# Kernel optimization log

Hardware: AMD Instinct MI355X
Metric: run time of the kernel (lower is better)

## Reference

```python
import jax, jax.numpy as jnp
import numpy as np

N, E, D, T = 50000, 500000, 128, 4
EPS = 1e-5


def setup_inputs() -> dict:
    key = jax.random.key(0)
    ks = jax.random.split(key, 14)
    s = 1.0 / np.sqrt(D)
    return {
        "x": jax.random.normal(ks[0], (N, D), jnp.float32),
        "edge_index": jax.random.randint(ks[1], (2, E), 0, N, jnp.int32),
        "edge_type": jax.random.randint(ks[2], (E,), 0, T, jnp.int32),
        "edge_features": jax.random.normal(ks[3], (E, D), jnp.float32),
        # per-edge-type linear transforms (torch Linear equiv, [in, out] layout)
        "W_types": jax.random.uniform(ks[4], (T, D, D), jnp.float32, -s, s),
        "b_types": jax.random.uniform(ks[5], (T, D), jnp.float32, -s, s),
        # self-loop transform (BaseGNNLayer.transform)
        "W_self": jax.random.uniform(ks[6], (D, D), jnp.float32, -s, s),
        "b_self": jax.random.uniform(ks[7], (D,), jnp.float32, -s, s),
        # edge_processor MLP: Linear(D, D) -> ReLU -> Linear(D, D)
        "W_e1": jax.random.uniform(ks[8], (D, D), jnp.float32, -s, s),
        "b_e1": jax.random.uniform(ks[9], (D,), jnp.float32, -s, s),
        "W_e2": jax.random.uniform(ks[10], (D, D), jnp.float32, -s, s),
        "b_e2": jax.random.uniform(ks[11], (D,), jnp.float32, -s, s),
        # LayerNorm params
        "ln_g": jnp.ones((D,), jnp.float32),
        "ln_b": jnp.zeros((D,), jnp.float32),
    }


def reference(x, edge_index, edge_type, edge_features,
              W_types, b_types, W_self, b_self,
              W_e1, b_e1, W_e2, b_e2, ln_g, ln_b):
    row, col = edge_index[0], edge_index[1]
    x_col = x[col]  # [E, D] gather of source-node features
    num_types = W_types.shape[0]
    # per-edge-type linear transform, selected by edge_type mask
    msgs = jnp.zeros((x_col.shape[0], W_types.shape[2]), x.dtype)
    for t in range(num_types):  # small fixed loop over edge types
        m_t = x_col @ W_types[t] + b_types[t]
        msgs = msgs + jnp.where((edge_type == t)[:, None], m_t, jnp.zeros((), x.dtype))
    # edge-feature MLP, added once per edge (each edge has exactly one type)
    ep = jax.nn.relu(edge_features @ W_e1 + b_e1) @ W_e2 + b_e2
    msgs = msgs + ep
    # scatter-add messages to destination nodes
    out = jax.ops.segment_sum(msgs, row, num_segments=x.shape[0])
    # self loops via the base transform
    out = out + x @ W_self + b_self
    # LayerNorm over feature dim
    mu = jnp.mean(out, axis=-1, keepdims=True)
    var = jnp.mean(jnp.square(out - mu), axis=-1, keepdims=True)
    out = (out - mu) * jax.lax.rsqrt(var + EPS) * ln_g + ln_b
    return jax.nn.relu(out)
```

## Files before the change

### kernel.cpp

```cpp
#include <hip/hip_runtime.h>

#define Nn 50000
#define Ee 500000
#define Dd 128

typedef __attribute__((ext_vector_type(8))) short bf16x8;
typedef __attribute__((ext_vector_type(4))) float f32x4;

__device__ inline unsigned short f2bf(float f) {
  unsigned u = __float_as_uint(f);
  unsigned r = u + 0x7FFFu + ((u >> 16) & 1u);
  return (unsigned short)(r >> 16);
}

__global__ __launch_bounds__(256) void prep_kernel(
    const float* __restrict__ x, const float* __restrict__ W_types,
    const float* __restrict__ b_types, const float* __restrict__ W_self,
    const float* __restrict__ W_e1, const float* __restrict__ W_e2,
    const float* __restrict__ b_e2,
    unsigned short* __restrict__ xbf, unsigned short* __restrict__ WTt,
    unsigned short* __restrict__ W1T, unsigned short* __restrict__ W2T,
    unsigned short* __restrict__ WsT, float* __restrict__ biasc) {
  int i = blockIdx.x * 256 + threadIdx.x;
  if (i < 65536) {
    int t = i >> 14, rem = i & 16383, n = rem >> 7, k = rem & 127;
    WTt[i] = f2bf(W_types[t * 16384 + k * 128 + n]);
  } else if (i < 81920) {
    int j = i - 65536; int n = j >> 7, k = j & 127;
    W1T[j] = f2bf(W_e1[k * 128 + n]);
  } else if (i < 98304) {
    int j = i - 81920; int n = j >> 7, k = j & 127;
    W2T[j] = f2bf(W_e2[k * 128 + n]);
  } else if (i < 114688) {
    int j = i - 98304; int n = j >> 7, k = j & 127;
    WsT[j] = f2bf(W_self[k * 128 + n]);
  } else if (i < 115200) {
    int j = i - 114688; int n = j & 127;
    biasc[j] = b_types[j] + b_e2[n];
  } else if (i < 115200 + Nn * Dd) {
    int j = i - 115200;
    xbf[j] = f2bf(x[j]);
  }
}

__global__ __launch_bounds__(256) void hist_kernel(const int* __restrict__ et,
                                                   int* __restrict__ hist) {
  __shared__ int h[4];
  if (threadIdx.x < 4) h[threadIdx.x] = 0;
  __syncthreads();
  for (int i = blockIdx.x * 256 + threadIdx.x; i < Ee; i += gridDim.x * 256)
    atomicAdd(&h[et[i]], 1);
  __syncthreads();
  if (threadIdx.x < 4) atomicAdd(&hist[threadIdx.x], h[threadIdx.x]);
}

__global__ void prefix_kernel(const int* __restrict__ hist, int* __restrict__ cursor) {
  if (threadIdx.x == 0) {
    int s = 0;
    for (int t = 0; t < 4; ++t) { cursor[t] = s; s += hist[t]; }
  }
}

__global__ __launch_bounds__(256) void scatter_kernel(const int* __restrict__ et,
                                                      int* __restrict__ cursor,
                                                      int* __restrict__ sorted_eid) {
  __shared__ int lc[4], bb[4];
  if (threadIdx.x < 4) lc[threadIdx.x] = 0;
  __syncthreads();
  int per = (Ee + gridDim.x - 1) / gridDim.x;
  int s = blockIdx.x * per;
  int e = min(Ee, s + per);
  for (int i = s + (int)threadIdx.x; i < e; i += 256) atomicAdd(&lc[et[i]], 1);
  __syncthreads();
  if (threadIdx.x < 4) bb[threadIdx.x] = atomicAdd(&cursor[threadIdx.x], lc[threadIdx.x]);
  __syncthreads();
  if (threadIdx.x < 4) lc[threadIdx.x] = bb[threadIdx.x];
  __syncthreads();
  for (int i = s + (int)threadIdx.x; i < e; i += 256) {
    int p = atomicAdd(&lc[et[i]], 1);
    sorted_eid[p] = i;
  }
}

__device__ inline void stageW(const unsigned short* __restrict__ Wg,
                              unsigned short* __restrict__ Wb, int tid) {
  const uint4* src = (const uint4*)Wg;
#pragma unroll
  for (int c = 0; c < 8; ++c) {
    int ch = c * 256 + tid;
    int row = ch >> 4;
    int off = (ch & 15) << 4;
    *(uint4*)((char*)Wb + row * 256 + (off ^ ((row & 7) << 4))) = src[ch];
  }
}

__global__ __launch_bounds__(256, 3) void edge_kernel(
    const int* __restrict__ edge_index, const int* __restrict__ edge_type,
    const float* __restrict__ ef, const unsigned short* __restrict__ xbf,
    const unsigned short* __restrict__ WTt, const unsigned short* __restrict__ W1T,
    const unsigned short* __restrict__ W2T, const float* __restrict__ biasc,
    const float* __restrict__ b_e1, const int* __restrict__ sorted_eid,
    float* __restrict__ accum) {
  __shared__ __align__(16) unsigned short Wb[16384];
  __shared__ unsigned short Hs[64][136];
  __shared__ int mrow[64];
  __shared__ int mtype[64];
  __shared__ int tmask_s;

  const int tid = threadIdx.x;
  const int tile0 = blockIdx.x * 64;

  if (tid < 64) {
    if (tid == 0) tmask_s = 0;
    int i = tile0 + tid;
    int r = -1, t = -1;
    if (i < Ee) {
      int ee = sorted_eid[i];
      r = edge_index[ee];
      t = edge_type[ee];
    }
    mrow[tid] = r;
    mtype[tid] = t;
    if (t >= 0) atomicOr(&tmask_s, 1 << t);
  }

  const int w = tid >> 6, l = tid & 63, quad = l >> 4, lm = l & 15;
  const int mr = w * 16 + lm;
  const int rswz = (lm & 7) << 4;

  const int i = tile0 + mr;
  const int e = sorted_eid[i < Ee ? i : Ee - 1];
  const int myt = edge_type[e];
  const int colnode = edge_index[Ee + e];

  bf16x8 ax[4];
  {
    const unsigned short* xp = xbf + colnode * Dd + quad * 8;
#pragma unroll
    for (int ks = 0; ks < 4; ++ks) ax[ks] = *(const bf16x8*)(xp + ks * 32);
  }

  stageW(W1T, Wb, tid);
  __syncthreads();

  f32x4 h[8];
#pragma unroll
  for (int c = 0; c < 8; ++c) h[c] = (f32x4){0.f, 0.f, 0.f, 0.f};
  const float* efp = ef + (long long)e * Dd + quad * 8;
#pragma unroll
  for (int ks = 0; ks < 4; ++ks) {
    float4 v0 = *(const float4*)(efp + ks * 32);
    float4 v1 = *(const float4*)(efp + ks * 32 + 4);
    bf16x8 a;
    a[0] = f2bf(v0.x); a[1] = f2bf(v0.y); a[2] = f2bf(v0.z); a[3] = f2bf(v0.w);
    a[4] = f2bf(v1.x); a[5] = f2bf(v1.y); a[6] = f2bf(v1.z); a[7] = f2bf(v1.w);
    const int fb = (ks * 64 + quad * 16) ^ rswz;
#pragma unroll
    for (int c = 0; c < 8; ++c) {
      bf16x8 b = *(const bf16x8*)((const char*)Wb + (c * 16 + lm) * 256 + fb);
      h[c] = __builtin_amdgcn_mfma_f32_16x16x32_bf16(a, b, h[c], 0, 0, 0);
    }
  }
#pragma unroll
  for (int c = 0; c < 8; ++c) {
    int n = c * 16 + lm;
    float be = b_e1[n];
#pragma unroll
    for (int r4 = 0; r4 < 4; ++r4) {
      float v = h[c][r4] + be;
      v = v > 0.f ? v : 0.f;
      Hs[w * 16 + quad * 4 + r4][n] = f2bf(v);
    }
  }
  __syncthreads();

  stageW(W2T, Wb, tid);
  __syncthreads();

  f32x4 msg[8];
#pragma unroll
  for (int c = 0; c < 8; ++c) msg[c] = (f32x4){0.f, 0.f, 0.f, 0.f};

#pragma unroll
  for (int ks = 0; ks < 4; ++ks) {
    bf16x8 a = *(const bf16x8*)&Hs[mr][ks * 32 + quad * 8];
    const int fb = (ks * 64 + quad * 16) ^ rswz;
#pragma unroll
    for (int c = 0; c < 8; ++c) {
      bf16x8 b = *(const bf16x8*)((const char*)Wb + (c * 16 + lm) * 256 + fb);
      msg[c] = __builtin_amdgcn_mfma_f32_16x16x32_bf16(a, b, msg[c], 0, 0, 0);
    }
  }
  __syncthreads();

  const int tmask = tmask_s;
  for (int t = 0; t < 4; ++t) {
    if (!(tmask & (1 << t))) continue;
    stageW(WTt + t * Dd * Dd, Wb, tid);
    __syncthreads();
    bool mine = (myt == t);
    if (__any(mine)) {
#pragma unroll
      for (int ks = 0; ks < 4; ++ks) {
        bf16x8 a = mine ? ax[ks] : (bf16x8){0, 0, 0, 0, 0, 0, 0, 0};
        const int fb = (ks * 64 + quad * 16) ^ rswz;
#pragma unroll
        for (int c = 0; c < 8; ++c) {
          bf16x8 b = *(const bf16x8*)((const char*)Wb + (c * 16 + lm) * 256 + fb);
          msg[c] = __builtin_amdgcn_mfma_f32_16x16x32_bf16(a, b, msg[c], 0, 0, 0);
        }
      }
    }
    __syncthreads();
  }

#pragma unroll
  for (int r4 = 0; r4 < 4; ++r4) {
    int m = w * 16 + quad * 4 + r4;
    int rn = mrow[m];
    if (rn < 0) continue;
    int t = mtype[m];
    float* dst = accum + (long long)rn * Dd;
    const float* bc = biasc + t * Dd;
#pragma unroll
    for (int c = 0; c < 8; ++c) {
      int n = c * 16 + lm;
      unsafeAtomicAdd(dst + n, msg[c][r4] + bc[n]);
    }
  }
}

__global__ __launch_bounds__(256) void selfln_kernel(
    const unsigned short* __restrict__ xbf, const unsigned short* __restrict__ WsT,
    const float* __restrict__ b_self, const float* __restrict__ accum,
    const float* __restrict__ ln_g, const float* __restrict__ ln_b,
    float* __restrict__ out) {
  __shared__ unsigned short Axl[64][136];
  __shared__ float S[64][132];
  __shared__ float P1[64][4], P2[64][4];
  __shared__ float MU[64], RS[64];

  const int tid = threadIdx.x;
  const int tile0 = blockIdx.x * 64;
  {
    const int r = tid >> 2, c0 = (tid & 3) * 32;
    int row = tile0 + r;
    if (row < Nn) {
      const uint4* xs = (const uint4*)(xbf + row * Dd + c0);
      uint4* xd = (uint4*)&Axl[r][c0];
      xd[0] = xs[0]; xd[1] = xs[1]; xd[2] = xs[2]; xd[3] = xs[3];
    } else {
      uint4 z = {0, 0, 0, 0};
      uint4* xd = (uint4*)&Axl[r][c0];
      xd[0] = z; xd[1] = z; xd[2] = z; xd[3] = z;
    }
  }
  __syncthreads();

  const int w = tid >> 6, l = tid & 63, quad = l >> 4, lm = l & 15;
  const int mr = w * 16 + lm;
  f32x4 acc[8];
#pragma unroll
  for (int c = 0; c < 8; ++c) acc[c] = (f32x4){0.f, 0.f, 0.f, 0.f};
#pragma unroll
  for (int ks = 0; ks < 4; ++ks) {
    bf16x8 a = *(const bf16x8*)&Axl[mr][ks * 32 + quad * 8];
#pragma unroll
    for (int c = 0; c < 8; ++c) {
      bf16x8 b = *(const bf16x8*)(WsT + (c * 16 + lm) * Dd + ks * 32 + quad * 8);
      acc[c] = __builtin_amdgcn_mfma_f32_16x16x32_bf16(a, b, acc[c], 0, 0, 0);
    }
  }
#pragma unroll
  for (int c = 0; c < 8; ++c) {
    int n = c * 16 + lm;
    float bs = b_self[n];
#pragma unroll
    for (int r4 = 0; r4 < 4; ++r4) {
      int m = w * 16 + quad * 4 + r4;
      int grow = tile0 + m;
      float v = acc[c][r4] + bs;
      if (grow < Nn) v += accum[(long long)grow * Dd + n];
      S[m][n] = v;
    }
  }
  __syncthreads();
  {
    const int r = tid >> 2, sgi = tid & 3, c0 = sgi * 32;
    float s1 = 0.f, s2 = 0.f;
#pragma unroll
    for (int j = 0; j < 32; ++j) { float v = S[r][c0 + j]; s1 += v; s2 += v * v; }
    P1[r][sgi] = s1; P2[r][sgi] = s2;
  }
  __syncthreads();
  if (tid < 64) {
    float s1 = P1[tid][0] + P1[tid][1] + P1[tid][2] + P1[tid][3];
    float s2 = P2[tid][0] + P2[tid][1] + P2[tid][2] + P2[tid][3];
    float mu = s1 * (1.f / 128.f);
    float var = s2 * (1.f / 128.f) - mu * mu;
    MU[tid] = mu;
    RS[tid] = rsqrtf(var + 1e-5f);
  }
  __syncthreads();
  {
    const int r = tid >> 2, c0 = (tid & 3) * 32;
    int row = tile0 + r;
    if (row < Nn) {
      float mu = MU[r], rs = RS[r];
      float* op = out + (long long)row * Dd + c0;
#pragma unroll
      for (int j = 0; j < 32; ++j) {
        float v = (S[r][c0 + j] - mu) * rs * ln_g[c0 + j] + ln_b[c0 + j];
        op[j] = v > 0.f ? v : 0.f;
      }
    }
  }
}

extern "C" void kernel_launch(void* const* d_in, const int* in_sizes, int n_in,
                              void* d_out, int out_size, void* d_ws, size_t ws_size,
                              hipStream_t stream) {
  (void)in_sizes; (void)n_in; (void)out_size; (void)ws_size;
  const float* x       = (const float*)d_in[0];
  const int*   eidx    = (const int*)d_in[1];
  const int*   etype   = (const int*)d_in[2];
  const float* ef      = (const float*)d_in[3];
  const float* W_types = (const float*)d_in[4];
  const float* b_types = (const float*)d_in[5];
  const float* W_self  = (const float*)d_in[6];
  const float* b_self  = (const float*)d_in[7];
  const float* W_e1    = (const float*)d_in[8];
  const float* b_e1    = (const float*)d_in[9];
  const float* W_e2    = (const float*)d_in[10];
  const float* b_e2    = (const float*)d_in[11];
  const float* ln_g    = (const float*)d_in[12];
  const float* ln_b    = (const float*)d_in[13];
  float* out = (float*)d_out;

  char* ws = (char*)d_ws;
  int*            ints   = (int*)ws;
  float*          accum  = (float*)(ws + 512);
  unsigned short* xbf    = (unsigned short*)(ws + 512 + 25600000);
  unsigned short* WTt    = (unsigned short*)(ws + 512 + 25600000 + 12800000);
  unsigned short* W1T    = WTt + 4 * 128 * 128;
  unsigned short* W2T    = W1T + 128 * 128;
  unsigned short* WsT    = W2T + 128 * 128;
  float*          biasc  = (float*)(WsT + 128 * 128);
  int*            sorted = (int*)((char*)biasc + 2048);

  hipMemsetAsync(ws, 0, 512 + (size_t)Nn * Dd * 4, stream);

  prep_kernel<<<25450, 256, 0, stream>>>(x, W_types, b_types, W_self, W_e1, W_e2,
                                         b_e2, xbf, WTt, W1T, W2T, WsT, biasc);
  hist_kernel<<<512, 256, 0, stream>>>(etype, ints);
  prefix_kernel<<<1, 64, 0, stream>>>(ints, ints + 4);
  scatter_kernel<<<512, 256, 0, stream>>>(etype, ints + 4, sorted);
  edge_kernel<<<(Ee + 63) / 64, 256, 0, stream>>>(eidx, etype, ef, xbf, WTt, W1T,
                                                  W2T, biasc, b_e1, sorted, accum);
  selfln_kernel<<<(Nn + 63) / 64, 256, 0, stream>>>(xbf, WsT, b_self, accum, ln_g,
                                                    ln_b, out);
}
```

Baseline: 700.2 us.

## Keep edge MLP hidden in registers via shuffles; register-only LayerNorm

The edge kernel now computes the first MLP layer transposed, so hidden activations land in a layout that wave shuffles can repack into A-fragments for the second layer. This removes the Hs shared buffer and its store/load round trip, and the edge-feature loads are issued early, before the weight staging. Occupancy bounds are raised from 3 to 4 blocks. The self/LayerNorm kernel moves to 128-thread, 32-row blocks and does the row reductions with in-wave xor shuffles instead of shared-memory passes. The cost is extra register pressure and shuffle instructions in exchange for less LDS traffic and fewer barriers.

Result: faster. 638.3 us (-8.9%).

```diff
diff --git a/kernel.cpp b/kernel.cpp
--- a/kernel.cpp
+++ b/kernel.cpp
@@ -94,7 +94,7 @@
   }
 }
 
-__global__ __launch_bounds__(256, 3) void edge_kernel(
+__global__ __launch_bounds__(256, 4) void edge_kernel(
     const int* __restrict__ edge_index, const int* __restrict__ edge_type,
     const float* __restrict__ ef, const unsigned short* __restrict__ xbf,
     const unsigned short* __restrict__ WTt, const unsigned short* __restrict__ W1T,
@@ -102,7 +102,6 @@
     const float* __restrict__ b_e1, const int* __restrict__ sorted_eid,
     float* __restrict__ accum) {
   __shared__ __align__(16) unsigned short Wb[16384];
-  __shared__ unsigned short Hs[64][136];
   __shared__ int mrow[64];
   __shared__ int mtype[64];
   __shared__ int tmask_s;
@@ -139,56 +138,77 @@
 #pragma unroll
     for (int ks = 0; ks < 4; ++ks) ax[ks] = *(const bf16x8*)(xp + ks * 32);
   }
+  float4 efr[8];
+  {
+    const float* efp = ef + (long long)e * Dd + quad * 8;
+#pragma unroll
+    for (int j = 0; j < 8; ++j)
+      efr[j] = *(const float4*)(efp + (j >> 1) * 32 + (j & 1) * 4);
+  }
 
   stageW(W1T, Wb, tid);
   __syncthreads();
 
-  f32x4 h[8];
-#pragma unroll
-  for (int c = 0; c < 8; ++c) h[c] = (f32x4){0.f, 0.f, 0.f, 0.f};
-  const float* efp = ef + (long long)e * Dd + quad * 8;
+  bf16x8 efrag[4];
 #pragma unroll
   for (int ks = 0; ks < 4; ++ks) {
-    float4 v0 = *(const float4*)(efp + ks * 32);
-    float4 v1 = *(const float4*)(efp + ks * 32 + 4);
+    float4 v0 = efr[2 * ks], v1 = efr[2 * ks + 1];
     bf16x8 a;
     a[0] = f2bf(v0.x); a[1] = f2bf(v0.y); a[2] = f2bf(v0.z); a[3] = f2bf(v0.w);
     a[4] = f2bf(v1.x); a[5] = f2bf(v1.y); a[6] = f2bf(v1.z); a[7] = f2bf(v1.w);
+    efrag[ks] = a;
+  }
+
+  f32x4 h2[8];
+#pragma unroll
+  for (int c = 0; c < 8; ++c) h2[c] = (f32x4){0.f, 0.f, 0.f, 0.f};
+#pragma unroll
+  for (int ks = 0; ks < 4; ++ks) {
     const int fb = (ks * 64 + quad * 16) ^ rswz;
 #pragma unroll
     for (int c = 0; c < 8; ++c) {
-      bf16x8 b = *(const bf16x8*)((const char*)Wb + (c * 16 + lm) * 256 + fb);
-      h[c] = __builtin_amdgcn_mfma_f32_16x16x32_bf16(a, b, h[c], 0, 0, 0);
-    }
-  }
+      bf16x8 wf = *(const bf16x8*)((const char*)Wb + (c * 16 + lm) * 256 + fb);
+      h2[c] = __builtin_amdgcn_mfma_f32_16x16x32_bf16(wf, efrag[ks], h2[c], 0, 0, 0);
+    }
+  }
+  __syncthreads();
+
+  stageW(W2T, Wb, tid);
+
+  int pk[8][2];
 #pragma unroll
   for (int c = 0; c < 8; ++c) {
-    int n = c * 16 + lm;
-    float be = b_e1[n];
-#pragma unroll
-    for (int r4 = 0; r4 < 4; ++r4) {
-      float v = h[c][r4] + be;
-      v = v > 0.f ? v : 0.f;
-      Hs[w * 16 + quad * 4 + r4][n] = f2bf(v);
-    }
-  }
-  __syncthreads();
-
-  stageW(W2T, Wb, tid);
+    float4 be = *(const float4*)(b_e1 + c * 16 + quad * 4);
+    float v0 = h2[c][0] + be.x; v0 = v0 > 0.f ? v0 : 0.f;
+    float v1 = h2[c][1] + be.y; v1 = v1 > 0.f ? v1 : 0.f;
+    float v2 = h2[c][2] + be.z; v2 = v2 > 0.f ? v2 : 0.f;
+    float v3 = h2[c][3] + be.w; v3 = v3 > 0.f ? v3 : 0.f;
+    pk[c][0] = (int)f2bf(v0) | ((int)f2bf(v1) << 16);
+    pk[c][1] = (int)f2bf(v2) | ((int)f2bf(v3) << 16);
+  }
   __syncthreads();
 
   f32x4 msg[8];
 #pragma unroll
   for (int c = 0; c < 8; ++c) msg[c] = (f32x4){0.f, 0.f, 0.f, 0.f};
 
+  const int sa = ((quad & 1) << 5) + lm;
+  const int sb = sa + 16;
+  const bool chi = ((quad >> 1) & 1) != 0;
 #pragma unroll
   for (int ks = 0; ks < 4; ++ks) {
-    bf16x8 a = *(const bf16x8*)&Hs[mr][ks * 32 + quad * 8];
+    int a0 = __shfl(pk[2 * ks][0], sa),     a1 = __shfl(pk[2 * ks][1], sa);
+    int a2 = __shfl(pk[2 * ks][0], sb),     a3 = __shfl(pk[2 * ks][1], sb);
+    int b0 = __shfl(pk[2 * ks + 1][0], sa), b1 = __shfl(pk[2 * ks + 1][1], sa);
+    int b2 = __shfl(pk[2 * ks + 1][0], sb), b3 = __shfl(pk[2 * ks + 1][1], sb);
+    union { int4 i; bf16x8 v; } cv;
+    cv.i = chi ? (int4){b0, b1, b2, b3} : (int4){a0, a1, a2, a3};
+    bf16x8 af = cv.v;
     const int fb = (ks * 64 + quad * 16) ^ rswz;
 #pragma unroll
     for (int c = 0; c < 8; ++c) {
-      bf16x8 b = *(const bf16x8*)((const char*)Wb + (c * 16 + lm) * 256 + fb);
-      msg[c] = __builtin_amdgcn_mfma_f32_16x16x32_bf16(a, b, msg[c], 0, 0, 0);
+      bf16x8 wf = *(const bf16x8*)((const char*)Wb + (c * 16 + lm) * 256 + fb);
+      msg[c] = __builtin_amdgcn_mfma_f32_16x16x32_bf16(af, wf, msg[c], 0, 0, 0);
     }
   }
   __syncthreads();
@@ -230,18 +250,15 @@
   }
 }
 
-__global__ __launch_bounds__(256) void selfln_kernel(
+__global__ __launch_bounds__(128, 4) void selfln_kernel(
     const unsigned short* __restrict__ xbf, const unsigned short* __restrict__ WsT,
     const float* __restrict__ b_self, const float* __restrict__ accum,
     const float* __restrict__ ln_g, const float* __restrict__ ln_b,
     float* __restrict__ out) {
-  __shared__ unsigned short Axl[64][136];
-  __shared__ float S[64][132];
-  __shared__ float P1[64][4], P2[64][4];
-  __shared__ float MU[64], RS[64];
+  __shared__ unsigned short Axl[32][136];
 
   const int tid = threadIdx.x;
-  const int tile0 = blockIdx.x * 64;
+  const int tile0 = blockIdx.x * 32;
   {
     const int r = tid >> 2, c0 = (tid & 3) * 32;
     int row = tile0 + r;
@@ -271,47 +288,47 @@
       acc[c] = __builtin_amdgcn_mfma_f32_16x16x32_bf16(a, b, acc[c], 0, 0, 0);
     }
   }
+
+  float s1[4] = {0.f, 0.f, 0.f, 0.f}, s2[4] = {0.f, 0.f, 0.f, 0.f};
 #pragma unroll
   for (int c = 0; c < 8; ++c) {
     int n = c * 16 + lm;
     float bs = b_self[n];
 #pragma unroll
     for (int r4 = 0; r4 < 4; ++r4) {
-      int m = w * 16 + quad * 4 + r4;
-      int grow = tile0 + m;
+      int grow = tile0 + w * 16 + quad * 4 + r4;
       float v = acc[c][r4] + bs;
       if (grow < Nn) v += accum[(long long)grow * Dd + n];
-      S[m][n] = v;
-    }
-  }
-  __syncthreads();
-  {
-    const int r = tid >> 2, sgi = tid & 3, c0 = sgi * 32;
-    float s1 = 0.f, s2 = 0.f;
-#pragma unroll
-    for (int j = 0; j < 32; ++j) { float v = S[r][c0 + j]; s1 += v; s2 += v * v; }
-    P1[r][sgi] = s1; P2[r][sgi] = s2;
-  }
-  __syncthreads();
-  if (tid < 64) {
-    float s1 = P1[tid][0] + P1[tid][1] + P1[tid][2] + P1[tid][3];
-    float s2 = P2[tid][0] + P2[tid][1] + P2[tid][2] + P2[tid][3];
-    float mu = s1 * (1.f / 128.f);
-    float var = s2 * (1.f / 128.f) - mu * mu;
-    MU[tid] = mu;
-    RS[tid] = rsqrtf(var + 1e-5f);
-  }
-  __syncthreads();
-  {
-    const int r = tid >> 2, c0 = (tid & 3) * 32;
-    int row = tile0 + r;
-    if (row < Nn) {
-      float mu = MU[r], rs = RS[r];
-      float* op = out + (long long)row * Dd + c0;
-#pragma unroll
-      for (int j = 0; j < 32; ++j) {
-        float v = (S[r][c0 + j] - mu) * rs * ln_g[c0 + j] + ln_b[c0 + j];
-        op[j] = v > 0.f ? v : 0.f;
+      acc[c][r4] = v;
+      s1[r4] += v;
+      s2[r4] += v * v;
+    }
+  }
+#pragma unroll
+  for (int off = 1; off < 16; off <<= 1) {
+#pragma unroll
+    for (int r4 = 0; r4 < 4; ++r4) {
+      s1[r4] += __shfl_xor(s1[r4], off);
+      s2[r4] += __shfl_xor(s2[r4], off);
+    }
+  }
+  float mu[4], rs[4];
+#pragma unroll
+  for (int r4 = 0; r4 < 4; ++r4) {
+    mu[r4] = s1[r4] * (1.f / 128.f);
+    float var = s2[r4] * (1.f / 128.f) - mu[r4] * mu[r4];
+    rs[r4] = rsqrtf(var + 1e-5f);
+  }
+#pragma unroll
+  for (int c = 0; c < 8; ++c) {
+    int n = c * 16 + lm;
+    float g = ln_g[n], bb = ln_b[n];
+#pragma unroll
+    for (int r4 = 0; r4 < 4; ++r4) {
+      int grow = tile0 + w * 16 + quad * 4 + r4;
+      if (grow < Nn) {
+        float v = (acc[c][r4] - mu[r4]) * rs[r4] * g + bb;
+        out[(long long)grow * Dd + n] = v > 0.f ? v : 0.f;
       }
     }
   }
@@ -357,6 +374,6 @@
   scatter_kernel<<<512, 256, 0, stream>>>(etype, ints + 4, sorted);
   edge_kernel<<<(Ee + 63) / 64, 256, 0, stream>>>(eidx, etype, ef, xbf, WTt, W1T,
                                                   W2T, biasc, b_e1, sorted, accum);
-  selfln_kernel<<<(Nn + 63) / 64, 256, 0, stream>>>(xbf, WsT, b_self, accum, ln_g,
+  selfln_kernel<<<(Nn + 31) / 32, 128, 0, stream>>>(xbf, WsT, b_self, accum, ln_g,
                                                     ln_b, out);
 }
```
